# Kernel optimization log

Hardware: AMD Instinct MI355X
Metric: run time of the kernel (lower is better)

Reference implementation:

```python
import jax, jax.numpy as jnp
import numpy as np

NEG_SLOPE = 0.2  # PyG GATConv default


def _gat_layer(x, src, dst, W, a_src, a_dst, b, heads, concat):
    # x: [N, F_in], W: [F_in, H*C], a_src/a_dst: [H, C], b: [H*C] or [C]
    N = x.shape[0]
    h = (x @ W).reshape(N, heads, -1)                      # [N, H, C]
    s_n = jnp.sum(h * a_src, axis=-1)                      # [N, H] per-node src score
    d_n = jnp.sum(h * a_dst, axis=-1)                      # [N, H] per-node dst score
    e = jax.nn.leaky_relu(s_n[src] + d_n[dst], NEG_SLOPE)  # [E, H] edge logits
    # segment softmax over incoming edges of each destination node
    m = jax.ops.segment_max(e, dst, num_segments=N)        # [N, H]
    ex = jnp.exp(e - m[dst])                               # [E, H]
    denom = jax.ops.segment_sum(ex, dst, num_segments=N)   # [N, H]
    alpha = ex / denom[dst]                                # [E, H]
    out = jax.ops.segment_sum(h[src] * alpha[:, :, None], dst, num_segments=N)  # [N, H, C]
    if concat:
        out = out.reshape(N, -1)
    else:
        out = out.mean(axis=1)
    return out + b


def setup_inputs() -> dict:
    key = jax.random.key(0)
    ks = jax.random.split(key, 12)
    N, E = 50000, 800000
    F_in, Ch, H, F_out = 128, 32, 4, 64
    x = jax.random.normal(ks[0], (N, F_in), dtype=jnp.float32)
    edge_index = jax.random.randint(ks[1], (2, E), 0, N, dtype=jnp.int64)
    # layer 1 params (glorot-ish scale)
    W1 = jax.random.normal(ks[2], (F_in, H * Ch), dtype=jnp.float32) * (1.0 / np.sqrt(F_in))
    a1_src = jax.random.normal(ks[3], (H, Ch), dtype=jnp.float32) * (1.0 / np.sqrt(Ch))
    a1_dst = jax.random.normal(ks[4], (H, Ch), dtype=jnp.float32) * (1.0 / np.sqrt(Ch))
    b1 = jnp.zeros((H * Ch,), dtype=jnp.float32)
    # layer 2 params (heads=1)
    W2 = jax.random.normal(ks[5], (H * Ch, F_out), dtype=jnp.float32) * (1.0 / np.sqrt(H * Ch))
    a2_src = jax.random.normal(ks[6], (1, F_out), dtype=jnp.float32) * (1.0 / np.sqrt(F_out))
    a2_dst = jax.random.normal(ks[7], (1, F_out), dtype=jnp.float32) * (1.0 / np.sqrt(F_out))
    b2 = jnp.zeros((F_out,), dtype=jnp.float32)
    return {"x": x, "edge_index": edge_index, "drpt": 0,
            "W1": W1, "a1_src": a1_src, "a1_dst": a1_dst, "b1": b1,
            "W2": W2, "a2_src": a2_src, "a2_dst": a2_dst, "b2": b2}


def reference(x, edge_index, drpt, W1, a1_src, a1_dst, b1, W2, a2_src, a2_dst, b2):
    N = x.shape[0]
    # PyG GATConv adds self-loops by default
    loops = jnp.arange(N, dtype=edge_index.dtype)
    src = jnp.concatenate([edge_index[0], loops])
    dst = jnp.concatenate([edge_index[1], loops])
    h = _gat_layer(x, src, dst, W1, a1_src, a1_dst, b1, heads=4, concat=True)
    h = jax.nn.relu(h)
    # F.dropout with training=False (eval) is identity; drpt unused at inference
    out = _gat_layer(h, src, dst, W2, a2_src, a2_dst, b2, heads=1, concat=True)
    return out
```

## Files before the change

### kernel.cpp

```cpp
#include <hip/hip_runtime.h>
#include <hip/hip_fp16.h>


typedef _Float16 half8 __attribute__((ext_vector_type(8)));
typedef float f32x4 __attribute__((ext_vector_type(4)));

constexpr int BCAP = 8192;
constexpr int NTHB = 256;
constexpr int NBIN = 128;

__global__ __launch_bounds__(256) void prep_wt(const float* __restrict__ W1,
                                               const float* __restrict__ W2,
                                               _Float16* __restrict__ Wt1,
                                               _Float16* __restrict__ Wt2,
                                               int* __restrict__ gtot) {
    int i = blockIdx.x * blockDim.x + threadIdx.x;
    if (i < 128 * 128) {
        int c = i >> 7, k = i & 127;
        Wt1[i] = (_Float16)W1[k * 128 + c];
    } else if (i < 128 * 128 + 64 * 128) {
        int j = i - 128 * 128;
        int c = j >> 7, k = j & 127;
        Wt2[j] = (_Float16)W2[k * 64 + c];
    } else if (i < 128 * 128 + 64 * 128 + 256) {
        gtot[i - (128 * 128 + 64 * 128)] = 0;
    }
}

__global__ __launch_bounds__(256) void fused_bin_gemm1(
        const int* __restrict__ ei, int* __restrict__ gtot,
        int* __restrict__ offs, unsigned int* __restrict__ packed,
        int E, int nb, int Epb,
        const float* __restrict__ X, const _Float16* __restrict__ Wt,
        const float* __restrict__ a_src, const float* __restrict__ a_dst,
        _Float16* __restrict__ Yh, float* __restrict__ s,
        float* __restrict__ d, int N) {
    __shared__ __align__(16) char smem[27056];
    const int tid = threadIdx.x;

    if (blockIdx.x < NBIN) {
        int* cnt = (int*)smem;
        int* scn = cnt + 256;
        unsigned int* staged = (unsigned int*)(scn + 256);
        const int blk = blockIdx.x;
        const int e0  = blk * Epb;
        int ecnt = E - e0; ecnt = ecnt < 0 ? 0 : (ecnt > Epb ? Epb : ecnt);

        cnt[tid] = 0;
        __syncthreads();
        for (int k = tid; k < ecnt; k += 256)
            atomicAdd(&cnt[ei[E + e0 + k] >> 8], 1);
        __syncthreads();

        int v = cnt[tid];
        scn[tid] = v;
        __syncthreads();
        for (int off = 1; off < 256; off <<= 1) {
            int t = (tid >= off) ? scn[tid - off] : 0;
            __syncthreads();
            scn[tid] += t;
            __syncthreads();
        }
        const int sbase = scn[tid] - v;
        if (tid < nb + 1) offs[blk * (nb + 1) + tid] = sbase;
        if (tid < nb && v) atomicAdd(&gtot[tid], v);
        cnt[tid] = sbase;
        __syncthreads();

        for (int k = tid; k < ecnt; k += 256) {
            int src = ei[e0 + k], dst = ei[E + e0 + k];
            int pos = atomicAdd(&cnt[dst >> 8], 1);
            staged[pos] = ((unsigned)(dst & 255) << 16) | (unsigned)src;
        }
        __syncthreads();

        unsigned int* dstp = &packed[(size_t)blk * Epb];
        for (int k = tid; k < ecnt; k += 256)
            dstp[k] = staged[k];
        return;
    }

    constexpr int H = 4, NT = 8, TPH = 2, FOUT = 128;
    auto xs = (_Float16(*)[136])smem;
    const int row0 = (blockIdx.x - NBIN) * 64;

    for (int c = tid; c < 2048; c += 256) {
        int r = c >> 5, c4 = c & 31;
        float4 v = make_float4(0.f, 0.f, 0.f, 0.f);
        if (row0 + r < N)
            v = reinterpret_cast<const float4*>(X)[(size_t)(row0 + r) * 32 + c4];
        _Float16* p = &xs[r][c4 * 4];
        p[0] = (_Float16)v.x; p[1] = (_Float16)v.y;
        p[2] = (_Float16)v.z; p[3] = (_Float16)v.w;
    }
    __syncthreads();

    const int wid  = tid >> 6;
    const int lane = tid & 63;
    const int l15  = lane & 15;
    const int lg   = lane >> 4;

    f32x4 acc[NT];
    #pragma unroll
    for (int n = 0; n < NT; ++n) acc[n] = (f32x4){0.f, 0.f, 0.f, 0.f};

    const half8* WtV = reinterpret_cast<const half8*>(Wt);
    #pragma unroll
    for (int ks = 0; ks < 4; ++ks) {
        half8 a = *reinterpret_cast<const half8*>(&xs[wid * 16 + l15][ks * 32 + lg * 8]);
        #pragma unroll
        for (int n = 0; n < NT; ++n) {
            half8 b = WtV[(size_t)(n * 16 + l15) * 16 + ks * 4 + lg];
            acc[n] = __builtin_amdgcn_mfma_f32_16x16x32_f16(a, b, acc[n], 0, 0, 0);
        }
    }

    float av[NT], bv[NT];
    #pragma unroll
    for (int n = 0; n < NT; ++n) {
        av[n] = a_src[n * 16 + l15];
        bv[n] = a_dst[n * 16 + l15];
    }

    #pragma unroll
    for (int r = 0; r < 4; ++r) {
        int row = row0 + wid * 16 + lg * 4 + r;
        bool ok = row < N;
        if (ok) {
            #pragma unroll
            for (int n = 0; n < NT; ++n)
                Yh[(size_t)row * FOUT + n * 16 + l15] = (_Float16)acc[n][r];
        }
        #pragma unroll
        for (int h = 0; h < H; ++h) {
            float ls = 0.f, ld = 0.f;
            #pragma unroll
            for (int t = 0; t < TPH; ++t) {
                int n = h * TPH + t;
                ls = fmaf(acc[n][r], av[n], ls);
                ld = fmaf(acc[n][r], bv[n], ld);
            }
            #pragma unroll
            for (int m = 1; m < 16; m <<= 1) {
                ls += __shfl_xor(ls, m);
                ld += __shfl_xor(ld, m);
            }
            if (ok && l15 == h) {
                s[(size_t)row * H + h] = ls;
                d[(size_t)row * H + h] = ld;
            }
        }
    }
}

__global__ __launch_bounds__(256) void build_csr(const unsigned int* __restrict__ packed,
                                                 const int* __restrict__ gtot,
                                                 const int* __restrict__ offs,
                                                 unsigned short* __restrict__ csr,
                                                 int* __restrict__ row_end,
                                                 int N, int nb, int Epb) {
    __shared__ int deg[256];
    __shared__ int scn[256];
    __shared__ int rst[NBIN], ren[NBIN];
    __shared__ unsigned short lcsr[BCAP + 256];
    const int b   = blockIdx.x;
    const int tid = threadIdx.x;
    const int node = (b << 8) + tid;
    const bool real = node < N;

    int nodes_t = N - tid * NTHB;
    nodes_t = nodes_t < 0 ? 0 : (nodes_t > NTHB ? NTHB : nodes_t);
    int vall = (tid < nb) ? gtot[tid] + nodes_t : 0;
    scn[tid] = vall;
    __syncthreads();
    for (int off = 1; off < 256; off <<= 1) {
        int t = (tid >= off) ? scn[tid - off] : 0;
        __syncthreads();
        scn[tid] += t;
        __syncthreads();
    }
    int nodes_b = N - b * NTHB;
    nodes_b = nodes_b < 0 ? 0 : (nodes_b > NTHB ? NTHB : nodes_b);
    const int gb = scn[b] - gtot[b] - nodes_b;
    __syncthreads();

    if (tid < NBIN) {
        rst[tid] = offs[tid * (nb + 1) + b];
        ren[tid] = offs[tid * (nb + 1) + b + 1];
    }
    deg[tid] = real ? 1 : 0;
    __syncthreads();

    const int wv = tid >> 6, ln = tid & 63;
    for (int i = wv; i < NBIN; i += 4) {
        const unsigned int* pk = &packed[(size_t)i * Epb];
        int st = rst[i], en = ren[i];
        for (int k = st + ln; k < en; k += 64)
            atomicAdd(&deg[pk[k] >> 16], 1);
    }
    __syncthreads();

    int v = deg[tid];
    scn[tid] = v;
    __syncthreads();
    for (int off = 1; off < 256; off <<= 1) {
        int t = (tid >= off) ? scn[tid - off] : 0;
        __syncthreads();
        scn[tid] += t;
        __syncthreads();
    }
    const int incl  = scn[tid];
    const int start = incl - v;
    const int tot   = scn[255];
    __syncthreads();

    if (real) {
        lcsr[start] = (unsigned short)node;
        row_end[node] = gb + incl;
    }
    deg[tid] = start + (real ? 1 : 0);
    __syncthreads();

    for (int i = wv; i < NBIN; i += 4) {
        const unsigned int* pk = &packed[(size_t)i * Epb];
        int st = rst[i], en = ren[i];
        for (int k = st + ln; k < en; k += 64) {
            unsigned int p = pk[k];
            int pos = atomicAdd(&deg[p >> 16], 1);
            lcsr[pos] = (unsigned short)(p & 0xffffu);
        }
    }
    __syncthreads();

    for (int k = tid; k < tot; k += 256)
        csr[gb + k] = lcsr[k];
}

__global__ __launch_bounds__(256) void gemm_score2(const _Float16* __restrict__ X,
                                                   const _Float16* __restrict__ Wt,
                                                   const float* __restrict__ a_src,
                                                   const float* __restrict__ a_dst,
                                                   _Float16* __restrict__ Yh,
                                                   float* __restrict__ s,
                                                   float* __restrict__ d, int N) {
    constexpr int FOUT = 64, NT = 4;
    __shared__ _Float16 xs[64][136];
    const int tid  = threadIdx.x;
    const int row0 = blockIdx.x * 64;

    for (int c = tid; c < 1024; c += 256) {
        int r = c >> 4, c8 = c & 15;
        uint4 v = make_uint4(0, 0, 0, 0);
        if (row0 + r < N)
            v = reinterpret_cast<const uint4*>(X)[(size_t)(row0 + r) * 16 + c8];
        *reinterpret_cast<uint4*>(&xs[r][c8 * 8]) = v;
    }
    __syncthreads();

    const int wid  = tid >> 6;
    const int lane = tid & 63;
    const int l15  = lane & 15;
    const int lg   = lane >> 4;

    f32x4 acc[NT];
    #pragma unroll
    for (int n = 0; n < NT; ++n) acc[n] = (f32x4){0.f, 0.f, 0.f, 0.f};

    const half8* WtV = reinterpret_cast<const half8*>(Wt);
    #pragma unroll
    for (int ks = 0; ks < 4; ++ks) {
        half8 a = *reinterpret_cast<const half8*>(&xs[wid * 16 + l15][ks * 32 + lg * 8]);
        #pragma unroll
        for (int n = 0; n < NT; ++n) {
            half8 b = WtV[(size_t)(n * 16 + l15) * 16 + ks * 4 + lg];
            acc[n] = __builtin_amdgcn_mfma_f32_16x16x32_f16(a, b, acc[n], 0, 0, 0);
        }
    }

    float av[NT], bv[NT];
    #pragma unroll
    for (int n = 0; n < NT; ++n) {
        av[n] = a_src[n * 16 + l15];
        bv[n] = a_dst[n * 16 + l15];
    }

    #pragma unroll
    for (int r = 0; r < 4; ++r) {
        int row = row0 + wid * 16 + lg * 4 + r;
        bool ok = row < N;
        float ls = 0.f, ld = 0.f;
        #pragma unroll
        for (int n = 0; n < NT; ++n) {
            if (ok) Yh[(size_t)row * FOUT + n * 16 + l15] = (_Float16)acc[n][r];
            ls = fmaf(acc[n][r], av[n], ls);
            ld = fmaf(acc[n][r], bv[n], ld);
        }
        #pragma unroll
        for (int m = 1; m < 16; m <<= 1) {
            ls += __shfl_xor(ls, m);
            ld += __shfl_xor(ld, m);
        }
        if (ok && l15 == 0) {
            s[row] = ls;
            d[row] = ld;
        }
    }
}

__device__ __forceinline__ float edge_w(float x) {
    return __expf(x > 0.f ? x : 0.2f * x);
}

__device__ __forceinline__ void acc8(float* acc, uint4 r, float w) {
    const __half2* h2 = reinterpret_cast<const __half2*>(&r);
    #pragma unroll
    for (int j = 0; j < 4; ++j) {
        float2 f = __half22float2(h2[j]);
        acc[2 * j]     = fmaf(w, f.x, acc[2 * j]);
        acc[2 * j + 1] = fmaf(w, f.y, acc[2 * j + 1]);
    }
}

template<int H, int C, bool RELU, bool OUTH>
__global__ __launch_bounds__(256) void gat_gather(const unsigned short* __restrict__ csr,
                                                  const int* __restrict__ row_end,
                                                  const float* __restrict__ s,
                                                  const float* __restrict__ d,
                                                  const _Float16* __restrict__ hh,
                                                  const float* __restrict__ b,
                                                  void* __restrict__ outp, int N) {
    constexpr int CT = H * C;
    constexpr int G  = CT / 8;
    int t = blockIdx.x * blockDim.x + threadIdx.x;
    int node = t / G;
    int lane = t % G;
    if (node >= N) return;

    int start = node ? row_end[node - 1] : 0;
    int end   = row_end[node];

    int c0 = lane * 8;
    int head = c0 / C;
    float dn = d[(size_t)node * H + head];

    float acc[8] = {0.f, 0.f, 0.f, 0.f, 0.f, 0.f, 0.f, 0.f};
    float den = 0.f;

    for (int k = start; k < end; k += 8) {
        int idx[8];
        float sv[8];
        uint4 rr[8];
        #pragma unroll
        for (int j = 0; j < 8; ++j) {
            int kk = k + j;
            int kc = kk < end ? kk : end - 1;
            idx[j] = csr[kc];
            sv[j]  = s[(size_t)idx[j] * H + head];
        }
        #pragma unroll
        for (int j = 0; j < 8; ++j)
            rr[j] = *reinterpret_cast<const uint4*>(&hh[(size_t)idx[j] * CT + c0]);
        #pragma unroll
        for (int j = 0; j < 8; ++j) {
            float w = edge_w(sv[j] + dn);
            if (k + j >= end) w = 0.f;
            den += w;
            acc8(acc, rr[j], w);
        }
    }

    float inv = 1.f / den;
    float o[8];
    #pragma unroll
    for (int j = 0; j < 8; ++j) {
        o[j] = acc[j] * inv + b[c0 + j];
        if (RELU) o[j] = fmaxf(o[j], 0.f);
    }
    if constexpr (OUTH) {
        union { _Float16 h[8]; uint4 u; } pk;
        #pragma unroll
        for (int j = 0; j < 8; ++j) pk.h[j] = (_Float16)o[j];
        _Float16* out = (_Float16*)outp;
        *reinterpret_cast<uint4*>(&out[(size_t)node * CT + c0]) = pk.u;
    } else {
        float* out = (float*)outp;
        float4* op = reinterpret_cast<float4*>(&out[(size_t)node * CT + c0]);
        op[0] = make_float4(o[0], o[1], o[2], o[3]);
        op[1] = make_float4(o[4], o[5], o[6], o[7]);
    }
}

extern "C" void kernel_launch(void* const* d_in, const int* in_sizes, int n_in,
                              void* d_out, int out_size, void* d_ws, size_t ws_size,
                              hipStream_t stream) {
    const float* x      = (const float*)d_in[0];
    const int*   ei     = (const int*)d_in[1];
    const float* W1     = (const float*)d_in[3];
    const float* a1_src = (const float*)d_in[4];
    const float* a1_dst = (const float*)d_in[5];
    const float* b1     = (const float*)d_in[6];
    const float* W2     = (const float*)d_in[7];
    const float* a2_src = (const float*)d_in[8];
    const float* a2_dst = (const float*)d_in[9];
    const float* b2     = (const float*)d_in[10];

    const int N = in_sizes[0] / 128;
    const int E = in_sizes[1] / 2;
    const int NB = (N + NTHB - 1) / NTHB;
    const int Epb = (E + NBIN - 1) / NBIN;
    const int NG1 = (N + 63) / 64;
    float* out = (float*)d_out;

    float* f = (float*)d_ws;
    _Float16* h1h = (_Float16*)f;
    _Float16* x2h = (_Float16*)(f + (size_t)N * 64);
    unsigned int* packed = (unsigned int*)x2h;
    float* s1 = f + (size_t)N * 128;
    float* d1 = f + (size_t)N * 132;
    int*   row_end = (int*)(f + (size_t)N * 136);
    int*   gtot    = row_end + N;
    int*   offs    = gtot + 256;
    _Float16* Wt1  = (_Float16*)(offs + NBIN * (NB + 1));
    _Float16* Wt2  = Wt1 + 128 * 128;
    unsigned short* csr = (unsigned short*)(Wt2 + 64 * 128);
    _Float16* h2h = h1h;
    float* s2 = s1;
    float* d2 = d1;

    prep_wt<<<97, 256, 0, stream>>>(W1, W2, Wt1, Wt2, gtot);
    fused_bin_gemm1<<<NBIN + NG1, 256, 0, stream>>>(
        ei, gtot, offs, packed, E, NB, Epb,
        x, Wt1, a1_src, a1_dst, h1h, s1, d1, N);
    build_csr<<<NB, 256, 0, stream>>>(packed, gtot, offs, csr, row_end, N, NB, Epb);
    gat_gather<4, 32, true, true><<<(int)(((size_t)N * 16 + 255) / 256), 256, 0, stream>>>(
        csr, row_end, s1, d1, h1h, b1, x2h, N);
    gemm_score2<<<NG1, 256, 0, stream>>>(x2h, Wt2, a2_src, a2_dst, h2h, s2, d2, N);
    gat_gather<1, 64, false, false><<<(int)(((size_t)N * 8 + 255) / 256), 256, 0, stream>>>(
        csr, row_end, s2, d2, h2h, b2, out, N);
}
```

Measured before the change: 125.5 us.

## Precount edges per bucket and scatter binned edges contiguously before CSR build

A new counting pass tallies destination buckets per edge chunk, and a scan kernel computes global per-bucket, per-chunk base offsets. The binning kernel then scatters each edge directly into a bucket-contiguous array instead of chunk-local order. build_csr can therefore read one contiguous range per bucket rather than walking 128 sub-ranges and redoing a global scan. The cost is an extra read of the destination indices, two extra launches, and a binary search per edge during the scatter.

```diff
diff --git a/kernel.cpp b/kernel.cpp
--- a/kernel.cpp
+++ b/kernel.cpp
@@ -9,39 +9,100 @@
 constexpr int NTHB = 256;
 constexpr int NBIN = 128;
 
-__global__ __launch_bounds__(256) void prep_wt(const float* __restrict__ W1,
-                                               const float* __restrict__ W2,
-                                               _Float16* __restrict__ Wt1,
-                                               _Float16* __restrict__ Wt2,
-                                               int* __restrict__ gtot) {
-    int i = blockIdx.x * blockDim.x + threadIdx.x;
-    if (i < 128 * 128) {
-        int c = i >> 7, k = i & 127;
-        Wt1[i] = (_Float16)W1[k * 128 + c];
-    } else if (i < 128 * 128 + 64 * 128) {
-        int j = i - 128 * 128;
-        int c = j >> 7, k = j & 127;
-        Wt2[j] = (_Float16)W2[k * 64 + c];
-    } else if (i < 128 * 128 + 64 * 128 + 256) {
-        gtot[i - (128 * 128 + 64 * 128)] = 0;
+__global__ __launch_bounds__(256) void prep_count(const float* __restrict__ W1,
+                                                  const float* __restrict__ W2,
+                                                  _Float16* __restrict__ Wt1,
+                                                  _Float16* __restrict__ Wt2,
+                                                  const int* __restrict__ ei,
+                                                  int* __restrict__ cntT,
+                                                  int E, int Epb) {
+    const int tid = threadIdx.x;
+    if (blockIdx.x < 97) {
+        int i = blockIdx.x * 256 + tid;
+        if (i < 128 * 128) {
+            int c = i >> 7, k = i & 127;
+            Wt1[i] = (_Float16)W1[k * 128 + c];
+        } else if (i < 128 * 128 + 64 * 128) {
+            int j = i - 128 * 128;
+            int c = j >> 7, k = j & 127;
+            Wt2[j] = (_Float16)W2[k * 64 + c];
+        }
+        return;
+    }
+    __shared__ int cnt[256];
+    const int blk = blockIdx.x - 97;
+    const int e0  = blk * Epb;
+    int ecnt = E - e0; ecnt = ecnt < 0 ? 0 : (ecnt > Epb ? Epb : ecnt);
+    cnt[tid] = 0;
+    __syncthreads();
+    for (int k = tid; k < ecnt; k += 256)
+        atomicAdd(&cnt[ei[E + e0 + k] >> 8], 1);
+    __syncthreads();
+    cntT[blk * 256 + tid] = cnt[tid];
+}
+
+__global__ __launch_bounds__(256) void scan_k(const int* __restrict__ cntT,
+                                              int* __restrict__ pbase,
+                                              int* __restrict__ ebase,
+                                              int nb) {
+    __shared__ int col[256];
+    __shared__ int cs2[NBIN];
+    const int b = blockIdx.x, tid = threadIdx.x;
+
+    int v = 0;
+    for (int i = 0; i < NBIN; ++i) v += cntT[i * 256 + tid];
+    col[tid] = v;
+    __syncthreads();
+    for (int off = 1; off < 256; off <<= 1) {
+        int t = (tid >= off) ? col[tid - off] : 0;
+        __syncthreads();
+        col[tid] += t;
+        __syncthreads();
+    }
+    const int eb = b ? col[b - 1] : 0;
+
+    int cv = 0;
+    if (tid < NBIN) {
+        cv = cntT[tid * 256 + b];
+        cs2[tid] = cv;
+    }
+    __syncthreads();
+    for (int off = 1; off < NBIN; off <<= 1) {
+        int t = (tid >= off && tid < NBIN) ? cs2[tid - off] : 0;
+        __syncthreads();
+        if (tid < NBIN) cs2[tid] += t;
+        __syncthreads();
+    }
+    if (tid < NBIN)
+        pbase[b * NBIN + tid] = eb + cs2[tid] - cv;
+
+    if (b == 0) {
+        if (tid < nb) ebase[tid] = col[tid] - v;
+    }
+    __syncthreads();
+    if (b == 0) {
+        int tot = 0;
+        for (int i = 0; i < NBIN; ++i) tot += cntT[i * 256 + tid];
+        if (tid < nb) ebase[tid] = col[tid] - tot;
+        if (tid == 0) ebase[nb] = col[nb - 1];
     }
 }
 
 __global__ __launch_bounds__(256) void fused_bin_gemm1(
-        const int* __restrict__ ei, int* __restrict__ gtot,
-        int* __restrict__ offs, unsigned int* __restrict__ packed,
-        int E, int nb, int Epb,
+        const int* __restrict__ ei, const int* __restrict__ pbase,
+        unsigned int* __restrict__ packed2, int E, int nb, int Epb,
         const float* __restrict__ X, const _Float16* __restrict__ Wt,
         const float* __restrict__ a_src, const float* __restrict__ a_dst,
         _Float16* __restrict__ Yh, float* __restrict__ s,
         float* __restrict__ d, int N) {
-    __shared__ __align__(16) char smem[27056];
+    __shared__ __align__(16) char smem[28080];
     const int tid = threadIdx.x;
 
     if (blockIdx.x < NBIN) {
         int* cnt = (int*)smem;
         int* scn = cnt + 256;
-        unsigned int* staged = (unsigned int*)(scn + 256);
+        int* pbs = scn + 256;
+        unsigned int* staged = (unsigned int*)(pbs + 256);
         const int blk = blockIdx.x;
         const int e0  = blk * Epb;
         int ecnt = E - e0; ecnt = ecnt < 0 ? 0 : (ecnt > Epb ? Epb : ecnt);
@@ -61,10 +122,8 @@
             scn[tid] += t;
             __syncthreads();
         }
-        const int sbase = scn[tid] - v;
-        if (tid < nb + 1) offs[blk * (nb + 1) + tid] = sbase;
-        if (tid < nb && v) atomicAdd(&gtot[tid], v);
-        cnt[tid] = sbase;
+        pbs[tid] = (tid < nb) ? pbase[tid * NBIN + blk] : 0;
+        cnt[tid] = scn[tid] - v;
         __syncthreads();
 
         for (int k = tid; k < ecnt; k += 256) {
@@ -74,9 +133,16 @@
         }
         __syncthreads();
 
-        unsigned int* dstp = &packed[(size_t)blk * Epb];
-        for (int k = tid; k < ecnt; k += 256)
-            dstp[k] = staged[k];
+        for (int k = tid; k < ecnt; k += 256) {
+            int lo = 0, hi = nb - 1;
+            while (lo < hi) {
+                int mid = (lo + hi) >> 1;
+                if (scn[mid] > k) hi = mid; else lo = mid + 1;
+            }
+            int b = lo;
+            int rs = b ? scn[b - 1] : 0;
+            packed2[(size_t)pbs[b] + (k - rs)] = staged[k];
+        }
         return;
     }
 
@@ -153,51 +219,29 @@
     }
 }
 
-__global__ __launch_bounds__(256) void build_csr(const unsigned int* __restrict__ packed,
-                                                 const int* __restrict__ gtot,
-                                                 const int* __restrict__ offs,
+__global__ __launch_bounds__(256) void build_csr(const unsigned int* __restrict__ packed2,
+                                                 const int* __restrict__ ebase,
                                                  unsigned short* __restrict__ csr,
                                                  int* __restrict__ row_end,
-                                                 int N, int nb, int Epb) {
+                                                 int N) {
     __shared__ int deg[256];
     __shared__ int scn[256];
-    __shared__ int rst[NBIN], ren[NBIN];
     __shared__ unsigned short lcsr[BCAP + 256];
     const int b   = blockIdx.x;
     const int tid = threadIdx.x;
+    const int e0  = ebase[b];
+    const int ne  = ebase[b + 1] - e0;
+    int nbase = b * NTHB; if (nbase > N) nbase = N;
+    const int gb  = e0 + nbase;
     const int node = (b << 8) + tid;
     const bool real = node < N;
 
-    int nodes_t = N - tid * NTHB;
-    nodes_t = nodes_t < 0 ? 0 : (nodes_t > NTHB ? NTHB : nodes_t);
-    int vall = (tid < nb) ? gtot[tid] + nodes_t : 0;
-    scn[tid] = vall;
-    __syncthreads();
-    for (int off = 1; off < 256; off <<= 1) {
-        int t = (tid >= off) ? scn[tid - off] : 0;
-        __syncthreads();
-        scn[tid] += t;
-        __syncthreads();
-    }
-    int nodes_b = N - b * NTHB;
-    nodes_b = nodes_b < 0 ? 0 : (nodes_b > NTHB ? NTHB : nodes_b);
-    const int gb = scn[b] - gtot[b] - nodes_b;
-    __syncthreads();
-
-    if (tid < NBIN) {
-        rst[tid] = offs[tid * (nb + 1) + b];
-        ren[tid] = offs[tid * (nb + 1) + b + 1];
-    }
     deg[tid] = real ? 1 : 0;
     __syncthreads();
 
-    const int wv = tid >> 6, ln = tid & 63;
-    for (int i = wv; i < NBIN; i += 4) {
-        const unsigned int* pk = &packed[(size_t)i * Epb];
-        int st = rst[i], en = ren[i];
-        for (int k = st + ln; k < en; k += 64)
-            atomicAdd(&deg[pk[k] >> 16], 1);
-    }
+    const unsigned int* pk = packed2 + e0;
+    for (int k = tid; k < ne; k += 256)
+        atomicAdd(&deg[pk[k] >> 16], 1);
     __syncthreads();
 
     int v = deg[tid];
@@ -221,14 +265,10 @@
     deg[tid] = start + (real ? 1 : 0);
     __syncthreads();
 
-    for (int i = wv; i < NBIN; i += 4) {
-        const unsigned int* pk = &packed[(size_t)i * Epb];
-        int st = rst[i], en = ren[i];
-        for (int k = st + ln; k < en; k += 64) {
-            unsigned int p = pk[k];
-            int pos = atomicAdd(&deg[p >> 16], 1);
-            lcsr[pos] = (unsigned short)(p & 0xffffu);
-        }
+    for (int k = tid; k < ne; k += 256) {
+        unsigned int p = pk[k];
+        int pos = atomicAdd(&deg[p >> 16], 1);
+        lcsr[pos] = (unsigned short)(p & 0xffffu);
     }
     __syncthreads();
 
@@ -414,24 +454,26 @@
     float* f = (float*)d_ws;
     _Float16* h1h = (_Float16*)f;
     _Float16* x2h = (_Float16*)(f + (size_t)N * 64);
-    unsigned int* packed = (unsigned int*)x2h;
+    unsigned int* packed2 = (unsigned int*)x2h;
     float* s1 = f + (size_t)N * 128;
     float* d1 = f + (size_t)N * 132;
     int*   row_end = (int*)(f + (size_t)N * 136);
-    int*   gtot    = row_end + N;
-    int*   offs    = gtot + 256;
-    _Float16* Wt1  = (_Float16*)(offs + NBIN * (NB + 1));
+    int*   cntT    = row_end + N;
+    int*   pbase   = cntT + NBIN * 256;
+    int*   ebase   = pbase + NB * NBIN;
+    _Float16* Wt1  = (_Float16*)(ebase + 256);
     _Float16* Wt2  = Wt1 + 128 * 128;
     unsigned short* csr = (unsigned short*)(Wt2 + 64 * 128);
     _Float16* h2h = h1h;
     float* s2 = s1;
     float* d2 = d1;
 
-    prep_wt<<<97, 256, 0, stream>>>(W1, W2, Wt1, Wt2, gtot);
+    prep_count<<<97 + NBIN, 256, 0, stream>>>(W1, W2, Wt1, Wt2, ei, cntT, E, Epb);
+    scan_k<<<NB, 256, 0, stream>>>(cntT, pbase, ebase, NB);
     fused_bin_gemm1<<<NBIN + NG1, 256, 0, stream>>>(
-        ei, gtot, offs, packed, E, NB, Epb,
+        ei, pbase, packed2, E, NB, Epb,
         x, Wt1, a1_src, a1_dst, h1h, s1, d1, N);
-    build_csr<<<NB, 256, 0, stream>>>(packed, gtot, offs, csr, row_end, N, NB, Epb);
+    build_csr<<<NB, 256, 0, stream>>>(packed2, ebase, csr, row_end, N);
     gat_gather<4, 32, true, true><<<(int)(((size_t)N * 16 + 255) / 256), 256, 0, stream>>>(
         csr, row_end, s1, d1, h1h, b1, x2h, N);
     gemm_score2<<<NG1, 256, 0, stream>>>(x2h, Wt2, a2_src, a2_dst, h2h, s2, d2, N);
```

Result: slower. 137.5 us (+9.6%).

## Scatter binned edges into per-bucket padded regions instead of per-block segments

Applied to the files above, without the earlier changes.

The binning blocks now reserve space in a global per-destination-bucket region (capacity BCAP) with an atomic cursor, pad each block's run to a multiple of 16 with sentinel entries, and write it there directly. The CSR build kernel then reads one contiguous region per bucket instead of walking a 128-block offset table with strided segments. The number of binning blocks is doubled to 256 and the offsets table is removed. This trades sentinel padding and global atomics for contiguous, coalesced reads in build_csr. Buckets that overflow BCAP are clamped, which could overwrite data on skewed graphs.

```diff
diff --git a/kernel.cpp b/kernel.cpp
--- a/kernel.cpp
+++ b/kernel.cpp
@@ -7,13 +7,14 @@
 
 constexpr int BCAP = 8192;
 constexpr int NTHB = 256;
-constexpr int NBIN = 128;
+constexpr int NBIN = 256;
+constexpr unsigned SENT = 0xFFFFFFFFu;
 
 __global__ __launch_bounds__(256) void prep_wt(const float* __restrict__ W1,
                                                const float* __restrict__ W2,
                                                _Float16* __restrict__ Wt1,
                                                _Float16* __restrict__ Wt2,
-                                               int* __restrict__ gtot) {
+                                               int* __restrict__ gcur) {
     int i = blockIdx.x * blockDim.x + threadIdx.x;
     if (i < 128 * 128) {
         int c = i >> 7, k = i & 127;
@@ -22,37 +23,39 @@
         int j = i - 128 * 128;
         int c = j >> 7, k = j & 127;
         Wt2[j] = (_Float16)W2[k * 64 + c];
-    } else if (i < 128 * 128 + 64 * 128 + 256) {
-        gtot[i - (128 * 128 + 64 * 128)] = 0;
+    } else if (i < 128 * 128 + 64 * 128 + 512) {
+        gcur[i - (128 * 128 + 64 * 128)] = 0;
     }
 }
 
 __global__ __launch_bounds__(256) void fused_bin_gemm1(
-        const int* __restrict__ ei, int* __restrict__ gtot,
-        int* __restrict__ offs, unsigned int* __restrict__ packed,
+        const int* __restrict__ ei, int* __restrict__ gcur,
+        int* __restrict__ gtot, unsigned int* __restrict__ packed,
         int E, int nb, int Epb,
         const float* __restrict__ X, const _Float16* __restrict__ Wt,
         const float* __restrict__ a_src, const float* __restrict__ a_dst,
         _Float16* __restrict__ Yh, float* __restrict__ s,
         float* __restrict__ d, int N) {
-    __shared__ __align__(16) char smem[27056];
+    __shared__ __align__(16) char smem[17408];
     const int tid = threadIdx.x;
 
     if (blockIdx.x < NBIN) {
-        int* cnt = (int*)smem;
-        int* scn = cnt + 256;
-        unsigned int* staged = (unsigned int*)(scn + 256);
+        int* hist = (int*)smem;
+        int* scn  = hist + 256;
+        int* cur  = scn + 256;
+        int* gbs  = cur + 256;
+        unsigned int* staged = (unsigned int*)(gbs + 256);
         const int blk = blockIdx.x;
         const int e0  = blk * Epb;
         int ecnt = E - e0; ecnt = ecnt < 0 ? 0 : (ecnt > Epb ? Epb : ecnt);
 
-        cnt[tid] = 0;
+        hist[tid] = 0;
         __syncthreads();
         for (int k = tid; k < ecnt; k += 256)
-            atomicAdd(&cnt[ei[E + e0 + k] >> 8], 1);
-        __syncthreads();
-
-        int v = cnt[tid];
+            atomicAdd(&hist[ei[E + e0 + k] >> 8], 1);
+        __syncthreads();
+
+        int v = hist[tid];
         scn[tid] = v;
         __syncthreads();
         for (int off = 1; off < 256; off <<= 1) {
@@ -61,22 +64,33 @@
             scn[tid] += t;
             __syncthreads();
         }
-        const int sbase = scn[tid] - v;
-        if (tid < nb + 1) offs[blk * (nb + 1) + tid] = sbase;
-        if (tid < nb && v) atomicAdd(&gtot[tid], v);
-        cnt[tid] = sbase;
+        if (tid < nb && v) {
+            int pad = (v + 15) & ~15;
+            int b0  = atomicAdd(&gcur[tid], pad);
+            if (b0 > BCAP - pad) b0 = BCAP - pad;
+            gbs[tid] = b0;
+            atomicAdd(&gtot[tid], v);
+        }
+        cur[tid] = scn[tid] - v;
         __syncthreads();
 
         for (int k = tid; k < ecnt; k += 256) {
             int src = ei[e0 + k], dst = ei[E + e0 + k];
-            int pos = atomicAdd(&cnt[dst >> 8], 1);
+            int pos = atomicAdd(&cur[dst >> 8], 1);
             staged[pos] = ((unsigned)(dst & 255) << 16) | (unsigned)src;
         }
         __syncthreads();
 
-        unsigned int* dstp = &packed[(size_t)blk * Epb];
-        for (int k = tid; k < ecnt; k += 256)
-            dstp[k] = staged[k];
+        const int wv = tid >> 6, ln = tid & 63;
+        for (int b = wv; b < nb; b += 4) {
+            int len = hist[b];
+            if (!len) continue;
+            int rs  = scn[b] - len;
+            int pad = (len + 15) & ~15;
+            unsigned int* dp = &packed[(size_t)b * BCAP + gbs[b]];
+            for (int k = ln; k < pad; k += 64)
+                dp[k] = (k < len) ? staged[rs + k] : SENT;
+        }
         return;
     }
 
@@ -154,14 +168,13 @@
 }
 
 __global__ __launch_bounds__(256) void build_csr(const unsigned int* __restrict__ packed,
+                                                 const int* __restrict__ gcur,
                                                  const int* __restrict__ gtot,
-                                                 const int* __restrict__ offs,
                                                  unsigned short* __restrict__ csr,
                                                  int* __restrict__ row_end,
-                                                 int N, int nb, int Epb) {
+                                                 int N, int nb) {
     __shared__ int deg[256];
     __shared__ int scn[256];
-    __shared__ int rst[NBIN], ren[NBIN];
     __shared__ unsigned short lcsr[BCAP + 256];
     const int b   = blockIdx.x;
     const int tid = threadIdx.x;
@@ -182,21 +195,16 @@
     int nodes_b = N - b * NTHB;
     nodes_b = nodes_b < 0 ? 0 : (nodes_b > NTHB ? NTHB : nodes_b);
     const int gb = scn[b] - gtot[b] - nodes_b;
-    __syncthreads();
-
-    if (tid < NBIN) {
-        rst[tid] = offs[tid * (nb + 1) + b];
-        ren[tid] = offs[tid * (nb + 1) + b + 1];
-    }
+    int ext = gcur[b]; if (ext > BCAP) ext = BCAP;
+    __syncthreads();
+
     deg[tid] = real ? 1 : 0;
     __syncthreads();
 
-    const int wv = tid >> 6, ln = tid & 63;
-    for (int i = wv; i < NBIN; i += 4) {
-        const unsigned int* pk = &packed[(size_t)i * Epb];
-        int st = rst[i], en = ren[i];
-        for (int k = st + ln; k < en; k += 64)
-            atomicAdd(&deg[pk[k] >> 16], 1);
+    const unsigned int* pk = &packed[(size_t)b * BCAP];
+    for (int k = tid; k < ext; k += 256) {
+        unsigned int p = pk[k];
+        if (p != SENT) atomicAdd(&deg[p >> 16], 1);
     }
     __syncthreads();
 
@@ -221,14 +229,11 @@
     deg[tid] = start + (real ? 1 : 0);
     __syncthreads();
 
-    for (int i = wv; i < NBIN; i += 4) {
-        const unsigned int* pk = &packed[(size_t)i * Epb];
-        int st = rst[i], en = ren[i];
-        for (int k = st + ln; k < en; k += 64) {
-            unsigned int p = pk[k];
-            int pos = atomicAdd(&deg[p >> 16], 1);
-            lcsr[pos] = (unsigned short)(p & 0xffffu);
-        }
+    for (int k = tid; k < ext; k += 256) {
+        unsigned int p = pk[k];
+        if (p == SENT) continue;
+        int pos = atomicAdd(&deg[p >> 16], 1);
+        lcsr[pos] = (unsigned short)(p & 0xffffu);
     }
     __syncthreads();
 
@@ -418,20 +423,20 @@
     float* s1 = f + (size_t)N * 128;
     float* d1 = f + (size_t)N * 132;
     int*   row_end = (int*)(f + (size_t)N * 136);
-    int*   gtot    = row_end + N;
-    int*   offs    = gtot + 256;
-    _Float16* Wt1  = (_Float16*)(offs + NBIN * (NB + 1));
+    int*   gcur    = row_end + N;
+    int*   gtot    = gcur + 256;
+    _Float16* Wt1  = (_Float16*)(gtot + 256);
     _Float16* Wt2  = Wt1 + 128 * 128;
     unsigned short* csr = (unsigned short*)(Wt2 + 64 * 128);
     _Float16* h2h = h1h;
     float* s2 = s1;
     float* d2 = d1;
 
-    prep_wt<<<97, 256, 0, stream>>>(W1, W2, Wt1, Wt2, gtot);
+    prep_wt<<<98, 256, 0, stream>>>(W1, W2, Wt1, Wt2, gcur);
     fused_bin_gemm1<<<NBIN + NG1, 256, 0, stream>>>(
-        ei, gtot, offs, packed, E, NB, Epb,
+        ei, gcur, gtot, packed, E, NB, Epb,
         x, Wt1, a1_src, a1_dst, h1h, s1, d1, N);
-    build_csr<<<NB, 256, 0, stream>>>(packed, gtot, offs, csr, row_end, N, NB, Epb);
+    build_csr<<<NB, 256, 0, stream>>>(packed, gcur, gtot, csr, row_end, N, NB);
     gat_gather<4, 32, true, true><<<(int)(((size_t)N * 16 + 255) / 256), 256, 0, stream>>>(
         csr, row_end, s1, d1, h1h, b1, x2h, N);
     gemm_score2<<<NG1, 256, 0, stream>>>(x2h, Wt2, a2_src, a2_dst, h2h, s2, d2, N);
```

New measurement: 120.5 us. 3.9% less time.
